# Optimization experiments

Measured on AMD Instinct MI355X. Metric: run time of the kernel, lower is better.

The kernel has to match this reference:

```python
import jax, jax.numpy as jnp
import numpy as np

SCALE = 8.0  # cfg.TEST_SCALE (eval path)


def setup_inputs() -> dict:
    key = jax.random.key(0)
    ks = jax.random.split(key, 5)
    N, D, F, NC = 65536, 1024, 300, 81
    return {
        "x": jax.random.normal(ks[0], (N, D), dtype=jnp.float32),
        "W_cls": jax.random.normal(ks[1], (1, D), dtype=jnp.float32) * 0.01,
        "b_cls": jnp.zeros((1,), dtype=jnp.float32),
        "W_sem": jax.random.normal(ks[2], (F, D), dtype=jnp.float32) * 0.01,
        "b_sem": jnp.zeros((F,), dtype=jnp.float32),
        "W_bbox": jax.random.normal(ks[3], (NC * 4, D), dtype=jnp.float32) * 0.001,
        "b_bbox": jnp.zeros((NC * 4,), dtype=jnp.float32),
        "sem_matrix": jax.random.normal(ks[4], (NC - 1, F), dtype=jnp.float32),
    }


def reference(x, W_cls, b_cls, W_sem, b_sem, W_bbox, b_bbox, sem_matrix):
    # b_score: Linear(D, 1)
    b_score = x @ W_cls.T + b_cls                      # [N, 1]
    # sem: Linear(D, F)
    sem = x @ W_sem.T + b_sem                          # [N, F]
    # eval path: scale * L2-row-normalized semantic matrix
    sm = SCALE * sem_matrix / jnp.linalg.norm(sem_matrix, axis=1, keepdims=True)
    # the original per-class repeat/mul/sum loop == one GEMM
    cls_score = sem @ sm.T                             # [N, NC-1]
    scores = jnp.concatenate([b_score, cls_score], axis=1)  # [N, NC]
    bbox_deltas = x @ W_bbox.T + b_bbox                # [N, NC*4]
    return (scores, bbox_deltas)
```

## Files before the change

kernel.cpp:

```cpp
#include <hip/hip_runtime.h>
#include <hip/hip_bf16.h>
#include <stdint.h>

#define KDIM 1024
#define NPAD 416
#define NCOLS 405
#define SCORE_COLS 81
#define BBOX_COLS 324
#define NROWS 65536
#define FDIM 300
#define SLAB (NPAD * 32)


typedef short v8s __attribute__((ext_vector_type(8)));
typedef float v4f __attribute__((ext_vector_type(4)));

__device__ __forceinline__ uint16_t f2bf(float f) {
    union { float f; uint32_t u; } c; c.f = f;
    uint32_t r = c.u + 0x7FFFu + ((c.u >> 16) & 1u);
    return (uint16_t)(r >> 16);
}

__device__ __forceinline__ size_t wt_off(int row, int k) {
    return (size_t)(k >> 5) * SLAB + (size_t)row * 32 + (k & 31);
}

__global__ void fill_w(const float* __restrict__ Wcls, const float* __restrict__ bcls,
                       const float* __restrict__ Wbbox, const float* __restrict__ bbbox,
                       uint16_t* __restrict__ Wt, float* __restrict__ bt) {
    int idx = blockIdx.x * 256 + threadIdx.x;
    int row = idx >> 10, k = idx & 1023;
    if (!(row >= 1 && row < 81)) {
        float v;
        if (row == 0) v = Wcls[k];
        else if (row < 81 + BBOX_COLS) v = Wbbox[(size_t)(row - 81) * KDIM + k];
        else v = 0.f;
        Wt[wt_off(row, k)] = f2bf(v);
    }
    if (k == 0 && !(row >= 1 && row < 81)) {
        float b;
        if (row == 0) b = bcls[0];
        else if (row < 81 + BBOX_COLS) b = bbbox[row - 81];
        else b = 0.f;
        bt[row] = b;
    }
}

__global__ void fill_w_sem(const float* __restrict__ Wsem, const float* __restrict__ bsem,
                           const float* __restrict__ semm,
                           uint16_t* __restrict__ Wt, float* __restrict__ bt) {
    const int n = blockIdx.x;
    const int kq = blockIdx.y;
    const int tid = threadIdx.x;
    __shared__ float s_row[FDIM];
    __shared__ float red[256];
    __shared__ float s_scale, s_bdot;

    const float* sr = semm + (size_t)n * FDIM;
    float p = 0.f, pb = 0.f;
    for (int f = tid; f < FDIM; f += 256) {
        float v = sr[f];
        s_row[f] = v;
        p += v * v;
        pb += v * bsem[f];
    }
    red[tid] = p; __syncthreads();
    for (int s = 128; s > 0; s >>= 1) { if (tid < s) red[tid] += red[tid + s]; __syncthreads(); }
    float norm2 = red[0]; __syncthreads();
    red[tid] = pb; __syncthreads();
    for (int s = 128; s > 0; s >>= 1) { if (tid < s) red[tid] += red[tid + s]; __syncthreads(); }
    if (tid == 0) { s_scale = 8.0f / sqrtf(norm2); s_bdot = red[0]; }
    __syncthreads();
    const float scale = s_scale;
    if (kq == 0 && tid == 0) bt[1 + n] = scale * s_bdot;

    const int k = kq * 256 + tid;
    float acc = 0.f;
    #pragma unroll 8
    for (int f = 0; f < FDIM; ++f) acc += s_row[f] * Wsem[(size_t)f * KDIM + k];
    Wt[wt_off(1 + n, k)] = f2bf(scale * acc);
}

#define A_STRIDE 36
#define A_BUF_ELEMS (64 * A_STRIDE)
#define EPS_STRIDE 409
#define SMEM_BYTES (32 * EPS_STRIDE * 4)

__device__ __forceinline__ void stcvt(uint16_t* p, float4 av) {
    __hip_bfloat162 lo = __float22bfloat162_rn(make_float2(av.x, av.y));
    __hip_bfloat162 hi = __float22bfloat162_rn(make_float2(av.z, av.w));
    uint2 v; v.x = *(uint32_t*)&lo; v.y = *(uint32_t*)&hi;
    *(uint2*)p = v;
}

__global__ __launch_bounds__(512, 4) void gemm_fused(
        const float* __restrict__ x, const uint16_t* __restrict__ Wt,
        const float* __restrict__ bt, float* __restrict__ out) {
    const int tid = threadIdx.x;
    const int wave = tid >> 6, lane = tid & 63;
    const int quad = lane >> 4, l16 = lane & 15;
    const int mtile = blockIdx.x;
    const int NT = (wave < 6) ? 4 : (wave == 6 ? 2 : 0);

    __shared__ __align__(16) char smem[SMEM_BYTES];
    uint16_t* As = (uint16_t*)smem;

    const float* xb = x + (size_t)mtile * 64 * KDIM;
    const int colbase = wave * 64;

    v4f acc[4][4];
    #pragma unroll
    for (int mi = 0; mi < 4; ++mi)
        #pragma unroll
        for (int ni = 0; ni < 4; ++ni)
            acc[mi][ni] = v4f{0.f, 0.f, 0.f, 0.f};

    const int am = tid >> 3, akc = tid & 7;
    const float* aptr = xb + (size_t)am * KDIM + akc * 4;

    const uint16_t* bfrag[4];
    #pragma unroll
    for (int ni = 0; ni < 4; ++ni) {
        int t = wave * 4 + ni; if (t > 25) t = 25;
        bfrag[ni] = Wt + (size_t)(t * 16 + l16) * 32 + quad * 8;
    }

    v8s bcur[4];
    float4 av_n, av_nn;

    {
        float4 av0 = *(const float4*)aptr;
        av_n  = *(const float4*)(aptr + 32);
        av_nn = *(const float4*)(aptr + 64);
        #pragma unroll
        for (int ni = 0; ni < 4; ++ni) bcur[ni] = *(const v8s*)bfrag[ni];
        stcvt(As + am * A_STRIDE + akc * 4, av0);
        asm volatile("s_waitcnt lgkmcnt(0)" ::: "memory");
        __builtin_amdgcn_s_barrier();
        asm volatile("" ::: "memory");
    }

    int rb = 0;
    for (int kt = 0; kt < 29; ++kt) {
        const uint16_t* Ar = As + rb * A_BUF_ELEMS;
        v8s a0 = *(const v8s*)(Ar + (0 * 16 + l16) * A_STRIDE + quad * 8);
        v8s a1 = *(const v8s*)(Ar + (1 * 16 + l16) * A_STRIDE + quad * 8);
        v8s a2 = *(const v8s*)(Ar + (2 * 16 + l16) * A_STRIDE + quad * 8);
        v8s a3 = *(const v8s*)(Ar + (3 * 16 + l16) * A_STRIDE + quad * 8);
        stcvt(As + (rb ^ 1) * A_BUF_ELEMS + am * A_STRIDE + akc * 4, av_n);
        av_n = av_nn;
        const size_t nxt = (size_t)(kt + 1) * SLAB;
        #pragma unroll
        for (int ni = 0; ni < 4; ++ni) {
            acc[0][ni] = __builtin_amdgcn_mfma_f32_16x16x32_bf16(a0, bcur[ni], acc[0][ni], 0, 0, 0);
            acc[1][ni] = __builtin_amdgcn_mfma_f32_16x16x32_bf16(a1, bcur[ni], acc[1][ni], 0, 0, 0);
            acc[2][ni] = __builtin_amdgcn_mfma_f32_16x16x32_bf16(a2, bcur[ni], acc[2][ni], 0, 0, 0);
            acc[3][ni] = __builtin_amdgcn_mfma_f32_16x16x32_bf16(a3, bcur[ni], acc[3][ni], 0, 0, 0);
            bcur[ni] = *(const v8s*)(bfrag[ni] + nxt);
        }
        __builtin_amdgcn_sched_barrier(0);
        av_nn = *(const float4*)(aptr + (size_t)(kt + 3) * 32);
        asm volatile("s_waitcnt lgkmcnt(0)" ::: "memory");
        __builtin_amdgcn_s_barrier();
        asm volatile("" ::: "memory");
        rb ^= 1;
    }

    {
        const uint16_t* Ar = As + rb * A_BUF_ELEMS;
        v8s a0 = *(const v8s*)(Ar + (0 * 16 + l16) * A_STRIDE + quad * 8);
        v8s a1 = *(const v8s*)(Ar + (1 * 16 + l16) * A_STRIDE + quad * 8);
        v8s a2 = *(const v8s*)(Ar + (2 * 16 + l16) * A_STRIDE + quad * 8);
        v8s a3 = *(const v8s*)(Ar + (3 * 16 + l16) * A_STRIDE + quad * 8);
        stcvt(As + (rb ^ 1) * A_BUF_ELEMS + am * A_STRIDE + akc * 4, av_n);
        av_n = av_nn;
        const size_t nxt = (size_t)30 * SLAB;
        #pragma unroll
        for (int ni = 0; ni < 4; ++ni) {
            acc[0][ni] = __builtin_amdgcn_mfma_f32_16x16x32_bf16(a0, bcur[ni], acc[0][ni], 0, 0, 0);
            acc[1][ni] = __builtin_amdgcn_mfma_f32_16x16x32_bf16(a1, bcur[ni], acc[1][ni], 0, 0, 0);
            acc[2][ni] = __builtin_amdgcn_mfma_f32_16x16x32_bf16(a2, bcur[ni], acc[2][ni], 0, 0, 0);
            acc[3][ni] = __builtin_amdgcn_mfma_f32_16x16x32_bf16(a3, bcur[ni], acc[3][ni], 0, 0, 0);
            bcur[ni] = *(const v8s*)(bfrag[ni] + nxt);
        }
        asm volatile("s_waitcnt lgkmcnt(0)" ::: "memory");
        __builtin_amdgcn_s_barrier();
        asm volatile("" ::: "memory");
        rb ^= 1;
    }

    {
        const uint16_t* Ar = As + rb * A_BUF_ELEMS;
        v8s a0 = *(const v8s*)(Ar + (0 * 16 + l16) * A_STRIDE + quad * 8);
        v8s a1 = *(const v8s*)(Ar + (1 * 16 + l16) * A_STRIDE + quad * 8);
        v8s a2 = *(const v8s*)(Ar + (2 * 16 + l16) * A_STRIDE + quad * 8);
        v8s a3 = *(const v8s*)(Ar + (3 * 16 + l16) * A_STRIDE + quad * 8);
        stcvt(As + (rb ^ 1) * A_BUF_ELEMS + am * A_STRIDE + akc * 4, av_n);
        const size_t nxt = (size_t)31 * SLAB;
        #pragma unroll
        for (int ni = 0; ni < 4; ++ni) {
            acc[0][ni] = __builtin_amdgcn_mfma_f32_16x16x32_bf16(a0, bcur[ni], acc[0][ni], 0, 0, 0);
            acc[1][ni] = __builtin_amdgcn_mfma_f32_16x16x32_bf16(a1, bcur[ni], acc[1][ni], 0, 0, 0);
            acc[2][ni] = __builtin_amdgcn_mfma_f32_16x16x32_bf16(a2, bcur[ni], acc[2][ni], 0, 0, 0);
            acc[3][ni] = __builtin_amdgcn_mfma_f32_16x16x32_bf16(a3, bcur[ni], acc[3][ni], 0, 0, 0);
            bcur[ni] = *(const v8s*)(bfrag[ni] + nxt);
        }
        asm volatile("s_waitcnt lgkmcnt(0)" ::: "memory");
        __builtin_amdgcn_s_barrier();
        asm volatile("" ::: "memory");
        rb ^= 1;
    }

    {
        const uint16_t* Ar = As + rb * A_BUF_ELEMS;
        v8s a0 = *(const v8s*)(Ar + (0 * 16 + l16) * A_STRIDE + quad * 8);
        v8s a1 = *(const v8s*)(Ar + (1 * 16 + l16) * A_STRIDE + quad * 8);
        v8s a2 = *(const v8s*)(Ar + (2 * 16 + l16) * A_STRIDE + quad * 8);
        v8s a3 = *(const v8s*)(Ar + (3 * 16 + l16) * A_STRIDE + quad * 8);
        #pragma unroll
        for (int ni = 0; ni < 4; ++ni) {
            acc[0][ni] = __builtin_amdgcn_mfma_f32_16x16x32_bf16(a0, bcur[ni], acc[0][ni], 0, 0, 0);
            acc[1][ni] = __builtin_amdgcn_mfma_f32_16x16x32_bf16(a1, bcur[ni], acc[1][ni], 0, 0, 0);
            acc[2][ni] = __builtin_amdgcn_mfma_f32_16x16x32_bf16(a2, bcur[ni], acc[2][ni], 0, 0, 0);
            acc[3][ni] = __builtin_amdgcn_mfma_f32_16x16x32_bf16(a3, bcur[ni], acc[3][ni], 0, 0, 0);
        }
    }

    const int rowbase = mtile * 64;
    float* eps = (float*)smem;
    float* outb = out + (size_t)NROWS * SCORE_COLS;
    float bias[4];
    #pragma unroll
    for (int ni = 0; ni < 4; ++ni)
        bias[ni] = (ni < NT) ? bt[colbase + ni * 16 + l16] : 0.f;
    #pragma unroll
    for (int h = 0; h < 2; ++h) {
        __syncthreads();
        #pragma unroll
        for (int mi2 = 0; mi2 < 2; ++mi2) {
            const int mi = h * 2 + mi2;
            #pragma unroll
            for (int ni = 0; ni < 4; ++ni) {
                const int col = colbase + ni * 16 + l16;
                if (ni < NT && col < NCOLS) {
                    #pragma unroll
                    for (int r = 0; r < 4; ++r)
                        eps[(mi2 * 16 + quad * 4 + r) * EPS_STRIDE + col] = acc[mi][ni][r] + bias[ni];
                }
            }
        }
        __syncthreads();
        const int row0 = rowbase + h * 32;
        for (int idx = tid; idx < 32 * SCORE_COLS; idx += 512) {
            int r = idx / SCORE_COLS, c = idx - r * SCORE_COLS;
            __builtin_nontemporal_store(eps[r * EPS_STRIDE + c],
                                        &out[(size_t)(row0 + r) * SCORE_COLS + c]);
        }
        for (int idx = tid; idx < 32 * BBOX_COLS; idx += 512) {
            int r = idx / BBOX_COLS, c = idx - r * BBOX_COLS;
            __builtin_nontemporal_store(eps[r * EPS_STRIDE + SCORE_COLS + c],
                                        &outb[(size_t)(row0 + r) * BBOX_COLS + c]);
        }
    }
}

extern "C" void kernel_launch(void* const* d_in, const int* in_sizes, int n_in,
                              void* d_out, int out_size, void* d_ws, size_t ws_size,
                              hipStream_t stream) {
    const float* x     = (const float*)d_in[0];
    const float* Wcls  = (const float*)d_in[1];
    const float* bcls  = (const float*)d_in[2];
    const float* Wsem  = (const float*)d_in[3];
    const float* bsem  = (const float*)d_in[4];
    const float* Wbbox = (const float*)d_in[5];
    const float* bbbox = (const float*)d_in[6];
    const float* semm  = (const float*)d_in[7];
    float* out = (float*)d_out;

    uint16_t* Wt = (uint16_t*)d_ws;
    float*    bt = (float*)((char*)d_ws + (size_t)NPAD * KDIM * 2);

    fill_w<<<dim3((NPAD * KDIM) / 256), dim3(256), 0, stream>>>(Wcls, bcls, Wbbox, bbbox, Wt, bt);
    fill_w_sem<<<dim3(80, 4), dim3(256), 0, stream>>>(Wsem, bsem, semm, Wt, bt);
    gemm_fused<<<dim3(NROWS / 64), dim3(512), 0, stream>>>(x, Wt, bt, out);
}
```

Before: 489.7 us.

## Shrink GEMM row tile to 32 and store results directly from registers

Reduces the block tile from 64 to 32 rows with 4 waves, each covering up to 7 interleaved 16-column tiles. The LDS-staged, coalesced nontemporal epilogue is replaced with direct per-element global stores. This cuts shared memory use and epilogue barriers, which may raise occupancy. In exchange, weight fragment reads per row double and output stores become strided and less coalesced.

```diff
diff --git a/kernel.cpp b/kernel.cpp
--- a/kernel.cpp
+++ b/kernel.cpp
@@ -81,10 +81,9 @@
     Wt[wt_off(1 + n, k)] = f2bf(scale * acc);
 }
 
+#define BM 32
 #define A_STRIDE 36
-#define A_BUF_ELEMS (64 * A_STRIDE)
-#define EPS_STRIDE 409
-#define SMEM_BYTES (32 * EPS_STRIDE * 4)
+#define A_BUF_ELEMS (BM * A_STRIDE)
 
 __device__ __forceinline__ void stcvt(uint16_t* p, float4 av) {
     __hip_bfloat162 lo = __float22bfloat162_rn(make_float2(av.x, av.y));
@@ -93,39 +92,37 @@
     *(uint2*)p = v;
 }
 
-__global__ __launch_bounds__(512, 4) void gemm_fused(
+__global__ __launch_bounds__(256, 4) void gemm_fused(
         const float* __restrict__ x, const uint16_t* __restrict__ Wt,
         const float* __restrict__ bt, float* __restrict__ out) {
     const int tid = threadIdx.x;
     const int wave = tid >> 6, lane = tid & 63;
     const int quad = lane >> 4, l16 = lane & 15;
     const int mtile = blockIdx.x;
-    const int NT = (wave < 6) ? 4 : (wave == 6 ? 2 : 0);
-
-    __shared__ __align__(16) char smem[SMEM_BYTES];
-    uint16_t* As = (uint16_t*)smem;
-
-    const float* xb = x + (size_t)mtile * 64 * KDIM;
-    const int colbase = wave * 64;
-
-    v4f acc[4][4];
+    const int NT = (wave < 2) ? 7 : 6;
+
+    __shared__ __align__(16) uint16_t As[2][A_BUF_ELEMS];
+
+    const float* xb = x + (size_t)mtile * BM * KDIM;
+
+    v4f acc[2][7];
     #pragma unroll
-    for (int mi = 0; mi < 4; ++mi)
-        #pragma unroll
-        for (int ni = 0; ni < 4; ++ni)
+    for (int mi = 0; mi < 2; ++mi)
+        #pragma unroll
+        for (int ni = 0; ni < 7; ++ni)
             acc[mi][ni] = v4f{0.f, 0.f, 0.f, 0.f};
 
     const int am = tid >> 3, akc = tid & 7;
     const float* aptr = xb + (size_t)am * KDIM + akc * 4;
 
-    const uint16_t* bfrag[4];
+    const uint16_t* bfrag[7];
     #pragma unroll
-    for (int ni = 0; ni < 4; ++ni) {
-        int t = wave * 4 + ni; if (t > 25) t = 25;
+    for (int ni = 0; ni < 7; ++ni) {
+        int t = wave + 4 * ni; if (t > 25) t = 25;
         bfrag[ni] = Wt + (size_t)(t * 16 + l16) * 32 + quad * 8;
     }
 
-    v8s bcur[4];
+    v8s bcur[7];
     float4 av_n, av_nn;
 
     {
@@ -133,8 +130,9 @@
         av_n  = *(const float4*)(aptr + 32);
         av_nn = *(const float4*)(aptr + 64);
         #pragma unroll
-        for (int ni = 0; ni < 4; ++ni) bcur[ni] = *(const v8s*)bfrag[ni];
-        stcvt(As + am * A_STRIDE + akc * 4, av0);
+        for (int ni = 0; ni < 7; ++ni)
+            if (ni < NT) bcur[ni] = *(const v8s*)bfrag[ni];
+        stcvt(&As[0][am * A_STRIDE + akc * 4], av0);
         asm volatile("s_waitcnt lgkmcnt(0)" ::: "memory");
         __builtin_amdgcn_s_barrier();
         asm volatile("" ::: "memory");
@@ -142,21 +140,19 @@
 
     int rb = 0;
     for (int kt = 0; kt < 29; ++kt) {
-        const uint16_t* Ar = As + rb * A_BUF_ELEMS;
-        v8s a0 = *(const v8s*)(Ar + (0 * 16 + l16) * A_STRIDE + quad * 8);
-        v8s a1 = *(const v8s*)(Ar + (1 * 16 + l16) * A_STRIDE + quad * 8);
-        v8s a2 = *(const v8s*)(Ar + (2 * 16 + l16) * A_STRIDE + quad * 8);
-        v8s a3 = *(const v8s*)(Ar + (3 * 16 + l16) * A_STRIDE + quad * 8);
-        stcvt(As + (rb ^ 1) * A_BUF_ELEMS + am * A_STRIDE + akc * 4, av_n);
+        const uint16_t* Ar = &As[rb][0];
+        v8s a0 = *(const v8s*)(Ar + (0 * 16 + l16) * A_STRIDE + quad * 8);
+        v8s a1 = *(const v8s*)(Ar + (1 * 16 + l16) * A_STRIDE + quad * 8);
+        stcvt(&As[rb ^ 1][am * A_STRIDE + akc * 4], av_n);
         av_n = av_nn;
         const size_t nxt = (size_t)(kt + 1) * SLAB;
         #pragma unroll
-        for (int ni = 0; ni < 4; ++ni) {
-            acc[0][ni] = __builtin_amdgcn_mfma_f32_16x16x32_bf16(a0, bcur[ni], acc[0][ni], 0, 0, 0);
-            acc[1][ni] = __builtin_amdgcn_mfma_f32_16x16x32_bf16(a1, bcur[ni], acc[1][ni], 0, 0, 0);
-            acc[2][ni] = __builtin_amdgcn_mfma_f32_16x16x32_bf16(a2, bcur[ni], acc[2][ni], 0, 0, 0);
-            acc[3][ni] = __builtin_amdgcn_mfma_f32_16x16x32_bf16(a3, bcur[ni], acc[3][ni], 0, 0, 0);
-            bcur[ni] = *(const v8s*)(bfrag[ni] + nxt);
+        for (int ni = 0; ni < 7; ++ni) {
+            if (ni < NT) {
+                acc[0][ni] = __builtin_amdgcn_mfma_f32_16x16x32_bf16(a0, bcur[ni], acc[0][ni], 0, 0, 0);
+                acc[1][ni] = __builtin_amdgcn_mfma_f32_16x16x32_bf16(a1, bcur[ni], acc[1][ni], 0, 0, 0);
+                bcur[ni] = *(const v8s*)(bfrag[ni] + nxt);
+            }
         }
         __builtin_amdgcn_sched_barrier(0);
         av_nn = *(const float4*)(aptr + (size_t)(kt + 3) * 32);
@@ -167,21 +163,19 @@
     }
 
     {
-        const uint16_t* Ar = As + rb * A_BUF_ELEMS;
-        v8s a0 = *(const v8s*)(Ar + (0 * 16 + l16) * A_STRIDE + quad * 8);
-        v8s a1 = *(const v8s*)(Ar + (1 * 16 + l16) * A_STRIDE + quad * 8);
-        v8s a2 = *(const v8s*)(Ar + (2 * 16 + l16) * A_STRIDE + quad * 8);
-        v8s a3 = *(const v8s*)(Ar + (3 * 16 + l16) * A_STRIDE + quad * 8);
-        stcvt(As + (rb ^ 1) * A_BUF_ELEMS + am * A_STRIDE + akc * 4, av_n);
+        const uint16_t* Ar = &As[rb][0];
+        v8s a0 = *(const v8s*)(Ar + (0 * 16 + l16) * A_STRIDE + quad * 8);
+        v8s a1 = *(const v8s*)(Ar + (1 * 16 + l16) * A_STRIDE + quad * 8);
+        stcvt(&As[rb ^ 1][am * A_STRIDE + akc * 4], av_n);
         av_n = av_nn;
         const size_t nxt = (size_t)30 * SLAB;
         #pragma unroll
-        for (int ni = 0; ni < 4; ++ni) {
-            acc[0][ni] = __builtin_amdgcn_mfma_f32_16x16x32_bf16(a0, bcur[ni], acc[0][ni], 0, 0, 0);
-            acc[1][ni] = __builtin_amdgcn_mfma_f32_16x16x32_bf16(a1, bcur[ni], acc[1][ni], 0, 0, 0);
-            acc[2][ni] = __builtin_amdgcn_mfma_f32_16x16x32_bf16(a2, bcur[ni], acc[2][ni], 0, 0, 0);
-            acc[3][ni] = __builtin_amdgcn_mfma_f32_16x16x32_bf16(a3, bcur[ni], acc[3][ni], 0, 0, 0);
-            bcur[ni] = *(const v8s*)(bfrag[ni] + nxt);
+        for (int ni = 0; ni < 7; ++ni) {
+            if (ni < NT) {
+                acc[0][ni] = __builtin_amdgcn_mfma_f32_16x16x32_bf16(a0, bcur[ni], acc[0][ni], 0, 0, 0);
+                acc[1][ni] = __builtin_amdgcn_mfma_f32_16x16x32_bf16(a1, bcur[ni], acc[1][ni], 0, 0, 0);
+                bcur[ni] = *(const v8s*)(bfrag[ni] + nxt);
+            }
         }
         asm volatile("s_waitcnt lgkmcnt(0)" ::: "memory");
         __builtin_amdgcn_s_barrier();
@@ -190,20 +184,18 @@
     }
 
     {
-        const uint16_t* Ar = As + rb * A_BUF_ELEMS;
-        v8s a0 = *(const v8s*)(Ar + (0 * 16 + l16) * A_STRIDE + quad * 8);
-        v8s a1 = *(const v8s*)(Ar + (1 * 16 + l16) * A_STRIDE + quad * 8);
-        v8s a2 = *(const v8s*)(Ar + (2 * 16 + l16) * A_STRIDE + quad * 8);
-        v8s a3 = *(const v8s*)(Ar + (3 * 16 + l16) * A_STRIDE + quad * 8);
-        stcvt(As + (rb ^ 1) * A_BUF_ELEMS + am * A_STRIDE + akc * 4, av_n);
+        const uint16_t* Ar = &As[rb][0];
+        v8s a0 = *(const v8s*)(Ar + (0 * 16 + l16) * A_STRIDE + quad * 8);
+        v8s a1 = *(const v8s*)(Ar + (1 * 16 + l16) * A_STRIDE + quad * 8);
+        stcvt(&As[rb ^ 1][am * A_STRIDE + akc * 4], av_n);
         const size_t nxt = (size_t)31 * SLAB;
         #pragma unroll
-        for (int ni = 0; ni < 4; ++ni) {
-            acc[0][ni] = __builtin_amdgcn_mfma_f32_16x16x32_bf16(a0, bcur[ni], acc[0][ni], 0, 0, 0);
-            acc[1][ni] = __builtin_amdgcn_mfma_f32_16x16x32_bf16(a1, bcur[ni], acc[1][ni], 0, 0, 0);
-            acc[2][ni] = __builtin_amdgcn_mfma_f32_16x16x32_bf16(a2, bcur[ni], acc[2][ni], 0, 0, 0);
-            acc[3][ni] = __builtin_amdgcn_mfma_f32_16x16x32_bf16(a3, bcur[ni], acc[3][ni], 0, 0, 0);
-            bcur[ni] = *(const v8s*)(bfrag[ni] + nxt);
+        for (int ni = 0; ni < 7; ++ni) {
+            if (ni < NT) {
+                acc[0][ni] = __builtin_amdgcn_mfma_f32_16x16x32_bf16(a0, bcur[ni], acc[0][ni], 0, 0, 0);
+                acc[1][ni] = __builtin_amdgcn_mfma_f32_16x16x32_bf16(a1, bcur[ni], acc[1][ni], 0, 0, 0);
+                bcur[ni] = *(const v8s*)(bfrag[ni] + nxt);
+            }
         }
         asm volatile("s_waitcnt lgkmcnt(0)" ::: "memory");
         __builtin_amdgcn_s_barrier();
@@ -212,54 +204,37 @@
     }
 
     {
-        const uint16_t* Ar = As + rb * A_BUF_ELEMS;
-        v8s a0 = *(const v8s*)(Ar + (0 * 16 + l16) * A_STRIDE + quad * 8);
-        v8s a1 = *(const v8s*)(Ar + (1 * 16 + l16) * A_STRIDE + quad * 8);
-        v8s a2 = *(const v8s*)(Ar + (2 * 16 + l16) * A_STRIDE + quad * 8);
-        v8s a3 = *(const v8s*)(Ar + (3 * 16 + l16) * A_STRIDE + quad * 8);
-        #pragma unroll
-        for (int ni = 0; ni < 4; ++ni) {
-            acc[0][ni] = __builtin_amdgcn_mfma_f32_16x16x32_bf16(a0, bcur[ni], acc[0][ni], 0, 0, 0);
-            acc[1][ni] = __builtin_amdgcn_mfma_f32_16x16x32_bf16(a1, bcur[ni], acc[1][ni], 0, 0, 0);
-            acc[2][ni] = __builtin_amdgcn_mfma_f32_16x16x32_bf16(a2, bcur[ni], acc[2][ni], 0, 0, 0);
-            acc[3][ni] = __builtin_amdgcn_mfma_f32_16x16x32_bf16(a3, bcur[ni], acc[3][ni], 0, 0, 0);
-        }
-    }
-
-    const int rowbase = mtile * 64;
-    float* eps = (float*)smem;
+        const uint16_t* Ar = &As[rb][0];
+        v8s a0 = *(const v8s*)(Ar + (0 * 16 + l16) * A_STRIDE + quad * 8);
+        v8s a1 = *(const v8s*)(Ar + (1 * 16 + l16) * A_STRIDE + quad * 8);
+        #pragma unroll
+        for (int ni = 0; ni < 7; ++ni) {
+            if (ni < NT) {
+                acc[0][ni] = __builtin_amdgcn_mfma_f32_16x16x32_bf16(a0, bcur[ni], acc[0][ni], 0, 0, 0);
+                acc[1][ni] = __builtin_amdgcn_mfma_f32_16x16x32_bf16(a1, bcur[ni], acc[1][ni], 0, 0, 0);
+            }
+        }
+    }
+
+    const int rowbase = mtile * BM;
     float* outb = out + (size_t)NROWS * SCORE_COLS;
-    float bias[4];
     #pragma unroll
-    for (int ni = 0; ni < 4; ++ni)
-        bias[ni] = (ni < NT) ? bt[colbase + ni * 16 + l16] : 0.f;
-    #pragma unroll
-    for (int h = 0; h < 2; ++h) {
-        __syncthreads();
-        #pragma unroll
-        for (int mi2 = 0; mi2 < 2; ++mi2) {
-            const int mi = h * 2 + mi2;
-            #pragma unroll
-            for (int ni = 0; ni < 4; ++ni) {
-                const int col = colbase + ni * 16 + l16;
-                if (ni < NT && col < NCOLS) {
+    for (int ni = 0; ni < 7; ++ni) {
+        if (ni < NT) {
+            const int col = (wave + 4 * ni) * 16 + l16;
+            if (col < NCOLS) {
+                const float bb = bt[col];
+                float* base; int ldc, cc;
+                if (col < SCORE_COLS) { base = out;  ldc = SCORE_COLS; cc = col; }
+                else                  { base = outb; ldc = BBOX_COLS;  cc = col - SCORE_COLS; }
+                #pragma unroll
+                for (int mi = 0; mi < 2; ++mi)
                     #pragma unroll
-                    for (int r = 0; r < 4; ++r)
-                        eps[(mi2 * 16 + quad * 4 + r) * EPS_STRIDE + col] = acc[mi][ni][r] + bias[ni];
-                }
-            }
-        }
-        __syncthreads();
-        const int row0 = rowbase + h * 32;
-        for (int idx = tid; idx < 32 * SCORE_COLS; idx += 512) {
-            int r = idx / SCORE_COLS, c = idx - r * SCORE_COLS;
-            __builtin_nontemporal_store(eps[r * EPS_STRIDE + c],
-                                        &out[(size_t)(row0 + r) * SCORE_COLS + c]);
-        }
-        for (int idx = tid; idx < 32 * BBOX_COLS; idx += 512) {
-            int r = idx / BBOX_COLS, c = idx - r * BBOX_COLS;
-            __builtin_nontemporal_store(eps[r * EPS_STRIDE + SCORE_COLS + c],
-                                        &outb[(size_t)(row0 + r) * BBOX_COLS + c]);
+                    for (int r = 0; r < 4; ++r) {
+                        const int row = rowbase + mi * 16 + quad * 4 + r;
+                        base[(size_t)row * ldc + cc] = acc[mi][ni][r] + bb;
+                    }
+            }
         }
     }
 }
@@ -282,5 +257,5 @@
 
     fill_w<<<dim3((NPAD * KDIM) / 256), dim3(256), 0, stream>>>(Wcls, bcls, Wbbox, bbbox, Wt, bt);
     fill_w_sem<<<dim3(80, 4), dim3(256), 0, stream>>>(Wsem, bsem, semm, Wt, bt);
-    gemm_fused<<<dim3(NROWS / 64), dim3(512), 0, stream>>>(x, Wt, bt, out);
-}
+    gemm_fused<<<dim3(NROWS / BM), dim3(256), 0, stream>>>(x, Wt, bt, out);
+}
```

Measured after the change: 539.7 us. 1.1x slower.
